# Kernel tuning notes

Measured on AMD Instinct MI355X. Metric: run time of the kernel, lower is better.

## Reference

```python
import jax, jax.numpy as jnp
import numpy as np

AGENT_RADIUS = 0.5
SAFETY_DIST = 0.1
QP_ITERS = 300


def _qp_solve(p, G, h):
    """Batched QP: min_u 0.5 u^T u + p^T u  s.t.  G u <= h  (Q = I).
    Solved in the dual by projected gradient ascent (differentiable, fixed iters).
    p: [B,2], G: [B,m,2], h: [B,m] -> u: [B,2]
    """
    GGt = jnp.einsum('bmi,bni->bmn', G, G)                 # [B,m,m]
    q = jnp.einsum('bmi,bi->bm', G, p) + h                 # [B,m]
    # Lipschitz upper bound per sample (Frobenius norm of GG^T)
    L = jnp.sqrt(jnp.sum(GGt * GGt, axis=(1, 2))) + 1e-6   # [B]
    alpha = (1.0 / L)[:, None]

    def step(lam, _):
        grad = jnp.einsum('bmn,bn->bm', GGt, lam) + q
        lam = jnp.maximum(lam - alpha * grad, 0.0)
        return lam, None

    lam0 = jnp.zeros_like(h)
    lam, _ = jax.lax.scan(step, lam0, None, length=QP_ITERS)
    u = -p - jnp.einsum('bmi,bm->bi', G, lam)
    return u


def setup_inputs() -> dict:
    key = jax.random.key(0)
    ks = jax.random.split(key, 20)
    B, F, H1, H2 = 8192, 8, 1024, 512

    def w(k, i, o):
        return (jax.random.normal(k, (i, o), jnp.float32) / np.sqrt(i)).astype(jnp.float32)

    obs_xy = jax.random.uniform(ks[17], (8, 2), jnp.float32, -10.0, 10.0)
    obs_r = jax.random.uniform(ks[18], (8, 1), jnp.float32, 0.3, 0.8)
    return {
        'x': jax.random.normal(ks[0], (B, F), jnp.float32),
        'mean': 0.1 * jax.random.normal(ks[1], (F,), jnp.float32),
        'std': jax.random.uniform(ks[2], (F,), jnp.float32, 0.5, 1.5),
        'W1': w(ks[3], F, H1), 'b1': jnp.zeros((H1,), jnp.float32),
        'W21': w(ks[4], H1, H2), 'b21': jnp.zeros((H2,), jnp.float32),
        'W22': w(ks[5], H1, H2), 'b22': jnp.zeros((H2,), jnp.float32),
        'W23': w(ks[6], H1, H2), 'b23': jnp.zeros((H2,), jnp.float32),
        'W31': w(ks[7], H2, 2), 'b31': jnp.zeros((2,), jnp.float32),
        'W32': w(ks[8], H2, 2), 'b32': jnp.zeros((2,), jnp.float32),
        'W33': w(ks[9], H2, 1), 'b33': jnp.zeros((1,), jnp.float32),
        'obstacles': jnp.concatenate([obs_xy, obs_r], axis=1),  # [8,3] (x,y,r)
        'sgn': 1,
    }


def reference(x, mean, std, W1, b1, W21, b21, W22, b22, W23, b23,
              W31, b31, W32, b32, W33, b33, obstacles, sgn):
    B = x.shape[0]
    x0 = x * std + mean                                   # un-normalized state [B,8]

    h1 = jax.nn.relu(x @ W1 + b1)
    x21 = jax.nn.relu(h1 @ W21 + b21)
    x22 = jax.nn.relu(h1 @ W22 + b22)
    x23 = jax.nn.relu(h1 @ W23 + b23)
    x31 = x21 @ W31 + b31                                 # QP linear term p [B,2]
    x32 = 4.0 * jax.nn.sigmoid(x22 @ W32 + b32)           # CBF gains p1,p2 [B,2]
    x33 = 4.0 * jax.nn.sigmoid(x23 @ W33 + b33)           # liveness gain (unused, smg off)

    px, py, theta, v = x0[:, 0], x0[:, 1], x0[:, 2], x0[:, 3]
    st, ct = jnp.sin(theta)[:, None], jnp.cos(theta)[:, None]
    vb = v[:, None]

    # static obstacles broadcast to batch + opponent as last obstacle -> [B, m]
    ox = jnp.concatenate([jnp.broadcast_to(obstacles[:, 0][None], (B, obstacles.shape[0])), x0[:, 4:5]], axis=1)
    oy = jnp.concatenate([jnp.broadcast_to(obstacles[:, 1][None], (B, obstacles.shape[0])), x0[:, 5:6]], axis=1)
    orad = jnp.concatenate([jnp.broadcast_to(obstacles[:, 2][None], (B, obstacles.shape[0])),
                            jnp.full((B, 1), AGENT_RADIUS, x0.dtype)], axis=1)

    R = AGENT_RADIUS + orad + SAFETY_DIST
    dx = px[:, None] - ox                                  # [B,m]
    dy = py[:, None] - oy

    barrier = dx * dx + dy * dy - R * R
    barrier_dot = 2.0 * dx * vb * ct + 2.0 * dy * vb * st
    Lf2b = (2.0 * v * v)[:, None]
    LgLfbu1 = -2.0 * dx * vb * st + 2.0 * dy * vb * ct
    LgLfbu2 = 2.0 * dx * ct + 2.0 * dy * st
    G = jnp.stack([-LgLfbu1, -LgLfbu2], axis=-1)           # [B,m,2]
    p1, p2 = x32[:, 0:1], x32[:, 1:2]
    h = Lf2b + (p1 + p2) * barrier_dot + p1 * p2 * barrier # [B,m]

    u = _qp_solve(x31, G, h)                               # [B,2]
    return u
```

## Files before the change

### kernel.cpp

```cpp
#include <hip/hip_runtime.h>
#include <cstdint>
#include <cstddef>

typedef unsigned short u16;
typedef u16   u16x8  __attribute__((ext_vector_type(8)));
typedef u16   u16x4  __attribute__((ext_vector_type(4)));
typedef __bf16 bf16x8 __attribute__((ext_vector_type(8)));
typedef float f32x4  __attribute__((ext_vector_type(4)));
typedef float f32x2  __attribute__((ext_vector_type(2)));

__device__ __forceinline__ float bf2f(u16 v) {
  unsigned int u = ((unsigned int)v) << 16;
  return __builtin_bit_cast(float, u);
}
__device__ __forceinline__ u16 f2bf(float f) {
  unsigned int x = __builtin_bit_cast(unsigned int, f);
  x += 0x7fffu + ((x >> 16) & 1u);
  return (u16)(x >> 16);
}

__global__ __launch_bounds__(256) void k_tr(const float* __restrict__ W21,
                                            const float* __restrict__ W22,
                                            u16* __restrict__ Wt) {
  __shared__ u16 s[64][65];
  const int b   = blockIdx.x;
  const int mat = b >> 7;
  const int tt  = b & 127;
  const int k0  = (tt >> 3) * 64;
  const int n0  = (tt & 7) * 64;
  const float* W = mat ? W22 : W21;
  const int tx = threadIdx.x & 63;
  const int ty = threadIdx.x >> 6;
#pragma unroll
  for (int i = 0; i < 16; ++i) {
    int r = i * 4 + ty;
    s[r][tx] = f2bf(W[(size_t)(k0 + r) * 512 + n0 + tx]);
  }
  __syncthreads();
  const int nbase = mat * 512 + n0;
#pragma unroll
  for (int i = 0; i < 16; ++i) {
    int r = i * 4 + ty;
    Wt[(size_t)(nbase + r) * 1024 + k0 + tx] = s[tx][r];
  }
}

__global__ __launch_bounds__(256) void k_h1(const float* __restrict__ x,
                                            const float* __restrict__ W1,
                                            const float* __restrict__ b1,
                                            u16* __restrict__ h1) {
  const int row = blockIdx.x;
  const int c4  = threadIdx.x * 4;
  const float* xr = x + (size_t)row * 8;
  f32x4 acc = *(const f32x4*)(b1 + c4);
#pragma unroll
  for (int f = 0; f < 8; ++f) {
    float xv = xr[f];
    f32x4 wv = *(const f32x4*)(W1 + f * 1024 + c4);
#pragma unroll
    for (int e = 0; e < 4; ++e) acc[e] = fmaf(xv, wv[e], acc[e]);
  }
  u16x4 o;
#pragma unroll
  for (int e = 0; e < 4; ++e) o[e] = f2bf(fmaxf(acc[e], 0.f));
  *(u16x4*)(h1 + (size_t)row * 1024 + c4) = o;
}

__global__ __launch_bounds__(256) void k_gemm(const u16* __restrict__ A,
                                              const u16* __restrict__ Bt,
                                              const float* __restrict__ b21,
                                              const float* __restrict__ b22,
                                              u16* __restrict__ X2) {
  constexpr int K  = 1024;
  constexpr int BK = 32;
  constexpr int NT = K / BK;
  __shared__ u16 As[2][128 * BK];
  __shared__ u16 Bs[2][128 * BK];

  const int t    = threadIdx.x;
  const int row0 = blockIdx.y * 128;
  const int col0 = blockIdx.x * 128;
  const int w    = t >> 6;
  const int lane = t & 63;
  const int wr   = w >> 1, wc = w & 1;
  const int lrow = lane & 15;
  const int lk   = (lane >> 4) * 8;

  const int c0 = t, c1 = 256 + t;
  const u16* gA0 = A  + (size_t)(row0 + (c0 >> 2)) * K + (c0 & 3) * 8;
  const u16* gA1 = A  + (size_t)(row0 + (c1 >> 2)) * K + (c1 & 3) * 8;
  const u16* gB0 = Bt + (size_t)(col0 + (c0 >> 2)) * K + (c0 & 3) * 8;
  const u16* gB1 = Bt + (size_t)(col0 + (c1 >> 2)) * K + (c1 & 3) * 8;
  const int lo0 = c0 * 8, lo1 = c1 * 8;

  f32x4 acc[4][4];
#pragma unroll
  for (int i = 0; i < 4; ++i)
#pragma unroll
    for (int j = 0; j < 4; ++j) acc[i][j] = f32x4{0.f, 0.f, 0.f, 0.f};

  {
    u16x8 ta0 = *(const u16x8*)gA0;
    u16x8 ta1 = *(const u16x8*)gA1;
    u16x8 tb0 = *(const u16x8*)gB0;
    u16x8 tb1 = *(const u16x8*)gB1;
    *(u16x8*)(As[0] + lo0) = ta0;
    *(u16x8*)(As[0] + lo1) = ta1;
    *(u16x8*)(Bs[0] + lo0) = tb0;
    *(u16x8*)(Bs[0] + lo1) = tb1;
  }
  u16x8 na0 = *(const u16x8*)(gA0 + BK);
  u16x8 na1 = *(const u16x8*)(gA1 + BK);
  u16x8 nb0 = *(const u16x8*)(gB0 + BK);
  u16x8 nb1 = *(const u16x8*)(gB1 + BK);

  for (int kt = 0; kt < NT; ++kt) {
    const int cur = kt & 1, nxt = cur ^ 1;
    __syncthreads();

    const int koff = (kt + 2 < NT ? kt + 2 : NT - 1) * BK;
    u16x8 fa0 = *(const u16x8*)(gA0 + koff);
    u16x8 fa1 = *(const u16x8*)(gA1 + koff);
    u16x8 fb0 = *(const u16x8*)(gB0 + koff);
    u16x8 fb1 = *(const u16x8*)(gB1 + koff);

    bf16x8 af[4], bfr[4];
#pragma unroll
    for (int i = 0; i < 4; ++i)
      af[i] = __builtin_bit_cast(bf16x8,
          *(const u16x8*)(As[cur] + (wr * 64 + i * 16 + lrow) * BK + lk));
#pragma unroll
    for (int j = 0; j < 4; ++j)
      bfr[j] = __builtin_bit_cast(bf16x8,
          *(const u16x8*)(Bs[cur] + (wc * 64 + j * 16 + lrow) * BK + lk));
#pragma unroll
    for (int i = 0; i < 4; ++i)
#pragma unroll
      for (int j = 0; j < 4; ++j)
        acc[i][j] = __builtin_amdgcn_mfma_f32_16x16x32_bf16(af[i], bfr[j], acc[i][j], 0, 0, 0);

    if (kt + 1 < NT) {
      *(u16x8*)(As[nxt] + lo0) = na0;
      *(u16x8*)(As[nxt] + lo1) = na1;
      *(u16x8*)(Bs[nxt] + lo0) = nb0;
      *(u16x8*)(Bs[nxt] + lo1) = nb1;
    }
    na0 = fa0; na1 = fa1; nb0 = fb0; nb1 = fb1;
  }

#pragma unroll
  for (int j = 0; j < 4; ++j) {
    int col = col0 + wc * 64 + j * 16 + lrow;
    float bias = (col < 512) ? b21[col] : b22[col - 512];
#pragma unroll
    for (int i = 0; i < 4; ++i) {
      int rbase = row0 + wr * 64 + i * 16 + (lane >> 4) * 4;
#pragma unroll
      for (int rr = 0; rr < 4; ++rr) {
        float v = acc[i][j][rr] + bias;
        X2[(size_t)(rbase + rr) * 1024 + col] = f2bf(fmaxf(v, 0.f));
      }
    }
  }
}

__global__ __launch_bounds__(256) void k_head(const u16* __restrict__ X2,
                                              const float* __restrict__ W31,
                                              const float* __restrict__ W32,
                                              float* __restrict__ head) {
  const int wv   = threadIdx.x >> 6;
  const int lane = threadIdx.x & 63;
  const int r    = blockIdx.x * 4 + wv;
  const u16* row = X2 + (size_t)r * 1024;

  u16x8 v0 = *(const u16x8*)(row + lane * 8);
  u16x8 v1 = *(const u16x8*)(row + 512 + lane * 8);
  const f32x4* w31p = (const f32x4*)(W31 + lane * 16);
  const f32x4* w32p = (const f32x4*)(W32 + lane * 16);

  float a0x = 0.f, a0y = 0.f, a1x = 0.f, a1y = 0.f;
#pragma unroll
  for (int i = 0; i < 4; ++i) {
    f32x4 wa = w31p[i];
    float e0 = bf2f(v0[2 * i]), e1 = bf2f(v0[2 * i + 1]);
    a0x = fmaf(e0, wa[0], a0x); a0y = fmaf(e0, wa[1], a0y);
    a0x = fmaf(e1, wa[2], a0x); a0y = fmaf(e1, wa[3], a0y);
    f32x4 wb = w32p[i];
    float f0 = bf2f(v1[2 * i]), f1 = bf2f(v1[2 * i + 1]);
    a1x = fmaf(f0, wb[0], a1x); a1y = fmaf(f0, wb[1], a1y);
    a1x = fmaf(f1, wb[2], a1x); a1y = fmaf(f1, wb[3], a1y);
  }
#pragma unroll
  for (int m = 32; m >= 1; m >>= 1) {
    a0x += __shfl_xor(a0x, m, 64);
    a0y += __shfl_xor(a0y, m, 64);
    a1x += __shfl_xor(a1x, m, 64);
    a1y += __shfl_xor(a1y, m, 64);
  }
  if (lane == 0)
    *(f32x4*)(head + 4 * (size_t)r) = f32x4{a0x, a0y, a1x, a1y};
}

__global__ __launch_bounds__(64) void k_qp(const float* __restrict__ x,
                                           const float* __restrict__ mean_,
                                           const float* __restrict__ std_,
                                           const float* __restrict__ head,
                                           const float* __restrict__ b31,
                                           const float* __restrict__ b32,
                                           const float* __restrict__ obstacles,
                                           float* __restrict__ out) {
  const int r = blockIdx.x * 64 + threadIdx.x;
  f32x4 hd = *(const f32x4*)(head + 4 * (size_t)r);
  float p0  = hd[0] + b31[0];
  float p1v = hd[1] + b31[1];
  float pp1 = 4.f / (1.f + expf(-(hd[2] + b32[0])));
  float pp2 = 4.f / (1.f + expf(-(hd[3] + b32[1])));

  const f32x4* xp = (const f32x4*)(x + (size_t)r * 8);
  f32x4 xa = xp[0], xb = xp[1];
  float px = xa[0] * std_[0] + mean_[0];
  float py = xa[1] * std_[1] + mean_[1];
  float th = xa[2] * std_[2] + mean_[2];
  float v  = xa[3] * std_[3] + mean_[3];
  float ax = xb[0] * std_[4] + mean_[4];
  float ay = xb[1] * std_[5] + mean_[5];
  float st = sinf(th), ct = cosf(th);
  float Lf2b = 2.f * v * v;

  float G0[9], G1[9], q[9];
  float s00 = 0.f, s01 = 0.f, s11 = 0.f;
#pragma unroll
  for (int m = 0; m < 9; ++m) {
    float ox, oy, orad;
    if (m < 8) {
      ox = obstacles[m * 3]; oy = obstacles[m * 3 + 1]; orad = obstacles[m * 3 + 2];
    } else { ox = ax; oy = ay; orad = 0.5f; }
    float R  = 0.6f + orad;
    float dx = px - ox, dy = py - oy;
    float bar  = dx * dx + dy * dy - R * R;
    float dct  = dx * ct + dy * st;
    float bdot = 2.f * v * dct;
    float g0 = 2.f * v * (dx * st - dy * ct);
    float g1 = -2.f * dct;
    float h  = Lf2b + (pp1 + pp2) * bdot + pp1 * pp2 * bar;
    G0[m] = g0; G1[m] = g1;
    q[m] = g0 * p0 + g1 * p1v + h;
    s00 += g0 * g0; s01 += g0 * g1; s11 += g1 * g1;
  }
  float L = sqrtf(s00 * s00 + 2.f * s01 * s01 + s11 * s11) + 1e-6f;
  float alpha = 1.f / L;

  float lam[9];
#pragma unroll
  for (int m = 0; m < 9; ++m) lam[m] = 0.f;
  for (int it = 0; it < 300; ++it) {
    float pr0[9], pr1[9];
#pragma unroll
    for (int m = 0; m < 9; ++m) { pr0[m] = G0[m] * lam[m]; pr1[m] = G1[m] * lam[m]; }
    float t0 = (((pr0[0] + pr0[1]) + (pr0[2] + pr0[3])) +
                ((pr0[4] + pr0[5]) + (pr0[6] + pr0[7]))) + pr0[8];
    float t1 = (((pr1[0] + pr1[1]) + (pr1[2] + pr1[3])) +
                ((pr1[4] + pr1[5]) + (pr1[6] + pr1[7]))) + pr1[8];
#pragma unroll
    for (int m = 0; m < 9; ++m) {
      float g = fmaf(G0[m], t0, fmaf(G1[m], t1, q[m]));
      lam[m] = fmaxf(fmaf(-alpha, g, lam[m]), 0.f);
    }
  }
  float u0 = -p0, u1 = -p1v;
#pragma unroll
  for (int m = 0; m < 9; ++m) { u0 = fmaf(-G0[m], lam[m], u0); u1 = fmaf(-G1[m], lam[m], u1); }
  *(f32x2*)(out + 2 * (size_t)r) = f32x2{u0, u1};
}

extern "C" void kernel_launch(void* const* d_in, const int* in_sizes, int n_in,
                              void* d_out, int out_size, void* d_ws, size_t ws_size,
                              hipStream_t stream) {
  const float* x    = (const float*)d_in[0];
  const float* mean_= (const float*)d_in[1];
  const float* std_ = (const float*)d_in[2];
  const float* W1   = (const float*)d_in[3];
  const float* b1   = (const float*)d_in[4];
  const float* W21  = (const float*)d_in[5];
  const float* b21  = (const float*)d_in[6];
  const float* W22  = (const float*)d_in[7];
  const float* b22  = (const float*)d_in[8];
  const float* W31  = (const float*)d_in[11];
  const float* b31  = (const float*)d_in[12];
  const float* W32  = (const float*)d_in[13];
  const float* b32  = (const float*)d_in[14];
  const float* obst = (const float*)d_in[17];
  float* out = (float*)d_out;

  char* ws = (char*)d_ws;
  u16*   Wt   = (u16*)ws;
  u16*   h1   = (u16*)(ws + (size_t)(1 << 21));
  u16*   X2   = (u16*)(ws + (size_t)(1 << 21) + (size_t)(1 << 24));
  float* head = (float*)(ws + (size_t)(1 << 21) + 2 * (size_t)(1 << 24));

  k_tr  <<<256, 256, 0, stream>>>(W21, W22, Wt);
  k_h1  <<<8192, 256, 0, stream>>>(x, W1, b1, h1);
  k_gemm<<<dim3(8, 64), 256, 0, stream>>>(h1, Wt, b21, b22, X2);
  k_head<<<2048, 256, 0, stream>>>(X2, W31, W32, head);
  k_qp  <<<128, 64, 0, stream>>>(x, mean_, std_, head, b31, b32, obst, out);
}
```

Before: 171.0 us.

## Fuse head projection into GEMM epilogue with atomics; merge prep kernels

The GEMM epilogue now applies bias and ReLU, then multiplies directly by the W31/W32 head weights. It reduces across lanes with shuffles and accumulates into the head buffer with atomicAdd, so the bf16 X2 intermediate and the separate head kernel are gone. The weight transpose and the first-layer kernels are merged into one launch that also zeroes the head buffer. The QP kernel now uses 256-thread blocks. This removes the 16 MB X2 write and read plus two launches, at the cost of float atomics, nondeterministic summation order, and more epilogue register pressure.

```diff
diff --git a/kernel.cpp b/kernel.cpp
--- a/kernel.cpp
+++ b/kernel.cpp
@@ -19,58 +19,64 @@
   return (u16)(x >> 16);
 }
 
-__global__ __launch_bounds__(256) void k_tr(const float* __restrict__ W21,
-                                            const float* __restrict__ W22,
-                                            u16* __restrict__ Wt) {
+__global__ __launch_bounds__(256) void k_prep(const float* __restrict__ W21,
+                                              const float* __restrict__ W22,
+                                              u16* __restrict__ Wt,
+                                              const float* __restrict__ x,
+                                              const float* __restrict__ W1,
+                                              const float* __restrict__ b1,
+                                              u16* __restrict__ h1,
+                                              float* __restrict__ head) {
   __shared__ u16 s[64][65];
-  const int b   = blockIdx.x;
-  const int mat = b >> 7;
-  const int tt  = b & 127;
-  const int k0  = (tt >> 3) * 64;
-  const int n0  = (tt & 7) * 64;
-  const float* W = mat ? W22 : W21;
-  const int tx = threadIdx.x & 63;
-  const int ty = threadIdx.x >> 6;
-#pragma unroll
-  for (int i = 0; i < 16; ++i) {
-    int r = i * 4 + ty;
-    s[r][tx] = f2bf(W[(size_t)(k0 + r) * 512 + n0 + tx]);
-  }
-  __syncthreads();
-  const int nbase = mat * 512 + n0;
-#pragma unroll
-  for (int i = 0; i < 16; ++i) {
-    int r = i * 4 + ty;
-    Wt[(size_t)(nbase + r) * 1024 + k0 + tx] = s[tx][r];
-  }
-}
-
-__global__ __launch_bounds__(256) void k_h1(const float* __restrict__ x,
-                                            const float* __restrict__ W1,
-                                            const float* __restrict__ b1,
-                                            u16* __restrict__ h1) {
-  const int row = blockIdx.x;
-  const int c4  = threadIdx.x * 4;
-  const float* xr = x + (size_t)row * 8;
-  f32x4 acc = *(const f32x4*)(b1 + c4);
-#pragma unroll
-  for (int f = 0; f < 8; ++f) {
-    float xv = xr[f];
-    f32x4 wv = *(const f32x4*)(W1 + f * 1024 + c4);
-#pragma unroll
-    for (int e = 0; e < 4; ++e) acc[e] = fmaf(xv, wv[e], acc[e]);
-  }
-  u16x4 o;
-#pragma unroll
-  for (int e = 0; e < 4; ++e) o[e] = f2bf(fmaxf(acc[e], 0.f));
-  *(u16x4*)(h1 + (size_t)row * 1024 + c4) = o;
+  const int b = blockIdx.x;
+  if (b < 256) {
+    const int mat = b >> 7;
+    const int tt  = b & 127;
+    const int k0  = (tt >> 3) * 64;
+    const int n0  = (tt & 7) * 64;
+    const float* W = mat ? W22 : W21;
+    const int tx = threadIdx.x & 63;
+    const int ty = threadIdx.x >> 6;
+#pragma unroll
+    for (int i = 0; i < 16; ++i) {
+      int r = i * 4 + ty;
+      s[r][tx] = f2bf(W[(size_t)(k0 + r) * 512 + n0 + tx]);
+    }
+    __syncthreads();
+    const int nbase = mat * 512 + n0;
+#pragma unroll
+    for (int i = 0; i < 16; ++i) {
+      int r = i * 4 + ty;
+      Wt[(size_t)(nbase + r) * 1024 + k0 + tx] = s[tx][r];
+    }
+  } else {
+    const int row = b - 256;
+    if (threadIdx.x == 0)
+      *(f32x4*)(head + 4 * (size_t)row) = f32x4{0.f, 0.f, 0.f, 0.f};
+    const int c4 = threadIdx.x * 4;
+    const float* xr = x + (size_t)row * 8;
+    f32x4 acc = *(const f32x4*)(b1 + c4);
+#pragma unroll
+    for (int f = 0; f < 8; ++f) {
+      float xv = xr[f];
+      f32x4 wv = *(const f32x4*)(W1 + f * 1024 + c4);
+#pragma unroll
+      for (int e = 0; e < 4; ++e) acc[e] = fmaf(xv, wv[e], acc[e]);
+    }
+    u16x4 o;
+#pragma unroll
+    for (int e = 0; e < 4; ++e) o[e] = f2bf(fmaxf(acc[e], 0.f));
+    *(u16x4*)(h1 + (size_t)row * 1024 + c4) = o;
+  }
 }
 
 __global__ __launch_bounds__(256) void k_gemm(const u16* __restrict__ A,
                                               const u16* __restrict__ Bt,
                                               const float* __restrict__ b21,
                                               const float* __restrict__ b22,
-                                              u16* __restrict__ X2) {
+                                              const float* __restrict__ W31,
+                                              const float* __restrict__ W32,
+                                              float* __restrict__ head) {
   constexpr int K  = 1024;
   constexpr int BK = 32;
   constexpr int NT = K / BK;
@@ -148,68 +154,58 @@
     na0 = fa0; na1 = fa1; nb0 = fb0; nb1 = fb1;
   }
 
+  const bool isX21 = (col0 < 512);
+  const float* Wh  = isX21 ? W31 : W32;
+  const int   hoff = isX21 ? 0 : 2;
+
+  float hx[16], hy[16];
+#pragma unroll
+  for (int n = 0; n < 16; ++n) { hx[n] = 0.f; hy[n] = 0.f; }
 #pragma unroll
   for (int j = 0; j < 4; ++j) {
-    int col = col0 + wc * 64 + j * 16 + lrow;
-    float bias = (col < 512) ? b21[col] : b22[col - 512];
-#pragma unroll
-    for (int i = 0; i < 4; ++i) {
-      int rbase = row0 + wr * 64 + i * 16 + (lane >> 4) * 4;
+    int col  = col0 + wc * 64 + j * 16 + lrow;
+    int wcol = col & 511;
+    f32x2 wv = *(const f32x2*)(Wh + 2 * wcol);
+    float bias = isX21 ? b21[col] : b22[wcol];
+#pragma unroll
+    for (int i = 0; i < 4; ++i)
 #pragma unroll
       for (int rr = 0; rr < 4; ++rr) {
-        float v = acc[i][j][rr] + bias;
-        X2[(size_t)(rbase + rr) * 1024 + col] = f2bf(fmaxf(v, 0.f));
+        float v = fmaxf(acc[i][j][rr] + bias, 0.f);
+        hx[i * 4 + rr] = fmaf(v, wv[0], hx[i * 4 + rr]);
+        hy[i * 4 + rr] = fmaf(v, wv[1], hy[i * 4 + rr]);
       }
-    }
-  }
-}
-
-__global__ __launch_bounds__(256) void k_head(const u16* __restrict__ X2,
-                                              const float* __restrict__ W31,
-                                              const float* __restrict__ W32,
-                                              float* __restrict__ head) {
-  const int wv   = threadIdx.x >> 6;
-  const int lane = threadIdx.x & 63;
-  const int r    = blockIdx.x * 4 + wv;
-  const u16* row = X2 + (size_t)r * 1024;
-
-  u16x8 v0 = *(const u16x8*)(row + lane * 8);
-  u16x8 v1 = *(const u16x8*)(row + 512 + lane * 8);
-  const f32x4* w31p = (const f32x4*)(W31 + lane * 16);
-  const f32x4* w32p = (const f32x4*)(W32 + lane * 16);
-
-  float a0x = 0.f, a0y = 0.f, a1x = 0.f, a1y = 0.f;
-#pragma unroll
-  for (int i = 0; i < 4; ++i) {
-    f32x4 wa = w31p[i];
-    float e0 = bf2f(v0[2 * i]), e1 = bf2f(v0[2 * i + 1]);
-    a0x = fmaf(e0, wa[0], a0x); a0y = fmaf(e0, wa[1], a0y);
-    a0x = fmaf(e1, wa[2], a0x); a0y = fmaf(e1, wa[3], a0y);
-    f32x4 wb = w32p[i];
-    float f0 = bf2f(v1[2 * i]), f1 = bf2f(v1[2 * i + 1]);
-    a1x = fmaf(f0, wb[0], a1x); a1y = fmaf(f0, wb[1], a1y);
-    a1x = fmaf(f1, wb[2], a1x); a1y = fmaf(f1, wb[3], a1y);
-  }
-#pragma unroll
-  for (int m = 32; m >= 1; m >>= 1) {
-    a0x += __shfl_xor(a0x, m, 64);
-    a0y += __shfl_xor(a0y, m, 64);
-    a1x += __shfl_xor(a1x, m, 64);
-    a1y += __shfl_xor(a1y, m, 64);
-  }
-  if (lane == 0)
-    *(f32x4*)(head + 4 * (size_t)r) = f32x4{a0x, a0y, a1x, a1y};
-}
-
-__global__ __launch_bounds__(64) void k_qp(const float* __restrict__ x,
-                                           const float* __restrict__ mean_,
-                                           const float* __restrict__ std_,
-                                           const float* __restrict__ head,
-                                           const float* __restrict__ b31,
-                                           const float* __restrict__ b32,
-                                           const float* __restrict__ obstacles,
-                                           float* __restrict__ out) {
-  const int r = blockIdx.x * 64 + threadIdx.x;
+  }
+#pragma unroll
+  for (int m = 1; m <= 8; m <<= 1) {
+#pragma unroll
+    for (int n = 0; n < 16; ++n) {
+      hx[n] += __shfl_xor(hx[n], m, 64);
+      hy[n] += __shfl_xor(hy[n], m, 64);
+    }
+  }
+  if (lrow == 0) {
+    const int rq = (lane >> 4) * 4;
+#pragma unroll
+    for (int i = 0; i < 4; ++i)
+#pragma unroll
+      for (int rr = 0; rr < 4; ++rr) {
+        int row = row0 + wr * 64 + i * 16 + rq + rr;
+        atomicAdd(head + 4 * (size_t)row + hoff,     hx[i * 4 + rr]);
+        atomicAdd(head + 4 * (size_t)row + hoff + 1, hy[i * 4 + rr]);
+      }
+  }
+}
+
+__global__ __launch_bounds__(256) void k_qp(const float* __restrict__ x,
+                                            const float* __restrict__ mean_,
+                                            const float* __restrict__ std_,
+                                            const float* __restrict__ head,
+                                            const float* __restrict__ b31,
+                                            const float* __restrict__ b32,
+                                            const float* __restrict__ obstacles,
+                                            float* __restrict__ out) {
+  const int r = blockIdx.x * 256 + threadIdx.x;
   f32x4 hd = *(const f32x4*)(head + 4 * (size_t)r);
   float p0  = hd[0] + b31[0];
   float p1v = hd[1] + b31[1];
@@ -295,12 +291,9 @@
   char* ws = (char*)d_ws;
   u16*   Wt   = (u16*)ws;
   u16*   h1   = (u16*)(ws + (size_t)(1 << 21));
-  u16*   X2   = (u16*)(ws + (size_t)(1 << 21) + (size_t)(1 << 24));
-  float* head = (float*)(ws + (size_t)(1 << 21) + 2 * (size_t)(1 << 24));
-
-  k_tr  <<<256, 256, 0, stream>>>(W21, W22, Wt);
-  k_h1  <<<8192, 256, 0, stream>>>(x, W1, b1, h1);
-  k_gemm<<<dim3(8, 64), 256, 0, stream>>>(h1, Wt, b21, b22, X2);
-  k_head<<<2048, 256, 0, stream>>>(X2, W31, W32, head);
-  k_qp  <<<128, 64, 0, stream>>>(x, mean_, std_, head, b31, b32, obst, out);
-}
+  float* head = (float*)(ws + (size_t)(1 << 21) + (size_t)(1 << 24));
+
+  k_prep<<<256 + 8192, 256, 0, stream>>>(W21, W22, Wt, x, W1, b1, h1, head);
+  k_gemm<<<dim3(8, 64), 256, 0, stream>>>(h1, Wt, b21, b22, W31, W32, head);
+  k_qp  <<<32, 256, 0, stream>>>(x, mean_, std_, head, b31, b32, obst, out);
+}
```

After: 171.6 us. About the same (+0.3%).
